# Performance work log

Measured on AMD Instinct MI355X. Metric: run time of the kernel, lower is better.

## Reference

```python
import jax, jax.numpy as jnp
import numpy as np

D, N_T, N, N_H = 8, 2048, 64, 8
STD_E = 0.02
STD_Q = 0.02


def setup_inputs() -> dict:
    key = jax.random.key(0)
    k1, k2, k3 = jax.random.split(key, 3)
    r_prime = jax.random.normal(k1, (D, N_T, N), dtype=jnp.float32)
    Q = jax.random.normal(k2, (N_H, N, N), dtype=jnp.float32) * STD_Q
    E = jax.random.normal(k3, (N_H, N, N), dtype=jnp.float32) * STD_E
    return {"r_prime": r_prime, "Q": Q, "E": E}


def reference(r_prime, Q, E):
    # r_prime: (b=d, t=n_t, i=n); Q, E: (h, i, j)
    n_t = r_prime.shape[1]
    # Omega[b,h,t,u] = sum_ij r'[b,t,i] Q[h,i,j] r'[b,u,j]
    Qr = jnp.einsum('hij,buj->bhui', Q, r_prime)          # (b, h, u, i)
    Omega = jnp.einsum('bti,bhui->bhtu', r_prime, Qr)     # (b, h, t, u)
    # causal lower-triangular mask (t >= u)
    mask = jnp.tril(jnp.ones((n_t, n_t), dtype=r_prime.dtype))
    Omega = Omega * mask  # broadcast over (b, h)
    # r[b,t,i] = sum_{h,u,j} Omega[b,h,t,u] E[h,i,j] r'[b,u,j]
    Er = jnp.einsum('hij,buj->bhui', E, r_prime)          # (b, h, u, i)
    r = jnp.einsum('bhtu,bhui->bti', Omega, Er)           # (b, t, i)
    return r
```

## Files before the change

kernel.cpp:

```cpp
#include <hip/hip_runtime.h>

#define D_B 8
#define N_T 2048
#define NN  64
#define N_H 8
#define N_C 32
#define NP  72

typedef __bf16 bf16;
typedef bf16 bf16x8 __attribute__((ext_vector_type(8)));
typedef bf16 bf16x4 __attribute__((ext_vector_type(4)));
typedef float f32x4 __attribute__((ext_vector_type(4)));

static __device__ __forceinline__ f32x4 mfma16(bf16x8 a, bf16x8 b, f32x4 c) {
    return __builtin_amdgcn_mfma_f32_16x16x32_bf16(a, b, c, 0, 0, 0);
}

static __device__ __forceinline__ bf16x8 ldcvt8(const float* p) {
    const f32x4 v0 = *(const f32x4*)p;
    const f32x4 v1 = *(const f32x4*)(p + 4);
    bf16x8 r;
#pragma unroll
    for (int k = 0; k < 4; k++) { r[k] = (bf16)v0[k]; r[4 + k] = (bf16)v1[k]; }
    return r;
}

__global__ __launch_bounds__(256, 3) void k_dg(
    const float* __restrict__ rp, const float* __restrict__ Qm,
    const float* __restrict__ Em,
    bf16* __restrict__ dGq, bf16* __restrict__ Rbf,
    bf16* __restrict__ Qrd, bf16* __restrict__ Erd)
{
    __shared__ bf16 Rl[64 * NP];
    __shared__ bf16 Ql[64 * NP];
    __shared__ bf16 El[64 * NP];
    __shared__ bf16 QT[64 * NP];
    __shared__ bf16 ET[64 * NP];
    const int b = blockIdx.x, c = blockIdx.y, qt = blockIdx.z;
    const int tid = threadIdx.x;
    const int w = tid >> 6, l = tid & 63, q = l >> 4, l16 = l & 15;
    const int row = tid >> 2, col = (tid & 3) * 16;

    {
        const float* src = rp + ((size_t)b * N_T + c * 64 + row) * NN + col;
        const bf16x8 v0 = ldcvt8(src), v1 = ldcvt8(src + 8);
        *(bf16x8*)&Rl[row * NP + col] = v0;
        *(bf16x8*)&Rl[row * NP + col + 8] = v1;
        if (qt == 0) {
            bf16* d = Rbf + ((size_t)b * N_T + c * 64 + row) * NN + col;
            *(bf16x8*)d = v0;
            *(bf16x8*)(d + 8) = v1;
        }
    }
    __syncthreads();
    const bf16x8 a0 = *(const bf16x8*)&Rl[(w * 16 + l16) * NP + q * 8];
    const bf16x8 a1 = *(const bf16x8*)&Rl[(w * 16 + l16) * NP + 32 + q * 8];

    f32x4 dacc[4];
#pragma unroll
    for (int ns = 0; ns < 4; ns++) { f32x4 z = {0.f, 0.f, 0.f, 0.f}; dacc[ns] = z; }

    for (int hh = 0; hh < 2; hh++) {
        const int h = qt * 2 + hh;
        {
            const float* qs = Qm + (size_t)h * 4096 + row * 64 + col;
            const float* es = Em + (size_t)h * 4096 + row * 64 + col;
            *(bf16x8*)&Ql[row * NP + col]     = ldcvt8(qs);
            *(bf16x8*)&Ql[row * NP + col + 8] = ldcvt8(qs + 8);
            *(bf16x8*)&El[row * NP + col]     = ldcvt8(es);
            *(bf16x8*)&El[row * NP + col + 8] = ldcvt8(es + 8);
        }
        __syncthreads();
        const size_t tb = (((size_t)(b * N_C + c)) * N_H + h) * 4096;
#pragma unroll
        for (int ns = 0; ns < 4; ns++) {
            bf16x8 b0 = *(const bf16x8*)&Ql[(ns * 16 + l16) * NP + q * 8];
            bf16x8 b1 = *(const bf16x8*)&Ql[(ns * 16 + l16) * NP + 32 + q * 8];
            f32x4 z = {0.f, 0.f, 0.f, 0.f};
            f32x4 s = mfma16(a0, b0, z);
            s = mfma16(a1, b1, s);
            bf16x4 p;
#pragma unroll
            for (int r = 0; r < 4; r++) p[r] = (bf16)s[r];
#pragma unroll
            for (int r = 0; r < 4; r++)
                Qrd[tb + (w * 16 + q * 4 + r) * 64 + ns * 16 + l16] = p[r];
            *(bf16x4*)&QT[(ns * 16 + l16) * NP + w * 16 + q * 4] = p;
            b0 = *(const bf16x8*)&El[(ns * 16 + l16) * NP + q * 8];
            b1 = *(const bf16x8*)&El[(ns * 16 + l16) * NP + 32 + q * 8];
            f32x4 s2 = mfma16(a0, b0, z);
            s2 = mfma16(a1, b1, s2);
#pragma unroll
            for (int r = 0; r < 4; r++) p[r] = (bf16)s2[r];
            *(bf16x4*)&ET[(ns * 16 + l16) * NP + w * 16 + q * 4] = p;
        }
        __syncthreads();
        {
            const bf16x8 qa0 = *(const bf16x8*)&QT[(w * 16 + l16) * NP + q * 8];
            const bf16x8 qa1 = *(const bf16x8*)&QT[(w * 16 + l16) * NP + 32 + q * 8];
#pragma unroll
            for (int ns = 0; ns < 4; ns++) {
                const bf16x8 e0 = *(const bf16x8*)&ET[(ns * 16 + l16) * NP + q * 8];
                const bf16x8 e1 = *(const bf16x8*)&ET[(ns * 16 + l16) * NP + 32 + q * 8];
                dacc[ns] = mfma16(qa0, e0, dacc[ns]);
                dacc[ns] = mfma16(qa1, e1, dacc[ns]);
            }
        }
        {
            const bf16x8 v0 = *(const bf16x8*)&ET[row * NP + col];
            const bf16x8 v1 = *(const bf16x8*)&ET[row * NP + col + 8];
            bf16* d = Erd + tb + row * 64 + col;
            *(bf16x8*)d = v0;
            *(bf16x8*)(d + 8) = v1;
        }
        __syncthreads();
    }
#pragma unroll
    for (int ns = 0; ns < 4; ns++) {
        bf16x4 p;
#pragma unroll
        for (int r = 0; r < 4; r++) p[r] = (bf16)dacc[ns][r];
        *(bf16x4*)&QT[(ns * 16 + l16) * NP + w * 16 + q * 4] = p;
    }
    __syncthreads();
    {
        bf16* dst = dGq + (((size_t)(b * N_C + c)) * 4 + qt) * 4096 + row * 64 + col;
        *(bf16x8*)dst       = *(const bf16x8*)&QT[row * NP + col];
        *(bf16x8*)(dst + 8) = *(const bf16x8*)&QT[row * NP + col + 8];
    }
}

__global__ __launch_bounds__(256, 4) void k_fold(const bf16* __restrict__ dGq,
                                                 bf16* __restrict__ dG8)
{
    const int b = blockIdx.x, c = blockIdx.y;
    const size_t base = ((size_t)(b * N_C + c)) * 4 * 4096 + threadIdx.x * 16;
    float s[16];
#pragma unroll
    for (int k = 0; k < 16; k++) s[k] = 0.f;
#pragma unroll
    for (int qt = 0; qt < 4; qt++) {
        const bf16x8 v0 = *(const bf16x8*)(dGq + base + (size_t)qt * 4096);
        const bf16x8 v1 = *(const bf16x8*)(dGq + base + (size_t)qt * 4096 + 8);
#pragma unroll
        for (int k = 0; k < 8; k++) { s[k] += (float)v0[k]; s[8 + k] += (float)v1[k]; }
    }
    bf16x8 o0, o1;
#pragma unroll
    for (int k = 0; k < 8; k++) { o0[k] = (bf16)s[k]; o1[k] = (bf16)s[8 + k]; }
    bf16* dst = dG8 + (size_t)(b * N_C + c) * 4096 + threadIdx.x * 16;
    *(bf16x8*)dst = o0;
    *(bf16x8*)(dst + 8) = o1;
}

__global__ __launch_bounds__(256, 4) void k_out(
    const bf16* __restrict__ dG8, const bf16* __restrict__ Rbf,
    const bf16* __restrict__ Qrd, const bf16* __restrict__ Erd,
    float* __restrict__ out)
{
    __shared__ bf16 Gb[64 * NP];
    __shared__ bf16 Sl[4 * 16 * NP];
    __shared__ float Ob[32 * 65];
    const int b = blockIdx.x, c = blockIdx.y, half = blockIdx.z;
    const int tid = threadIdx.x;
    const int w = tid >> 6, l = tid & 63, q = l >> 4, l16 = l & 15;
    const int s = w & 1, g = w >> 1;

    {
        float run[16];
#pragma unroll
        for (int k = 0; k < 16; k++) run[k] = 0.f;
        const bf16* base = dG8 + (size_t)b * N_C * 4096 + tid * 16;
        for (int cp = 0; cp < c; cp++) {
            const bf16x8 v0 = *(const bf16x8*)(base + (size_t)cp * 4096);
            const bf16x8 v1 = *(const bf16x8*)(base + (size_t)cp * 4096 + 8);
#pragma unroll
            for (int k = 0; k < 8; k++) { run[k] += (float)v0[k]; run[8 + k] += (float)v1[k]; }
        }
        bf16x8 o0, o1;
#pragma unroll
        for (int k = 0; k < 8; k++) { o0[k] = (bf16)run[k]; o1[k] = (bf16)run[8 + k]; }
        *(bf16x8*)&Gb[(tid >> 2) * NP + (tid & 3) * 16] = o0;
        *(bf16x8*)&Gb[(tid >> 2) * NP + (tid & 3) * 16 + 8] = o1;
    }
    __syncthreads();

    const int trow = c * 64 + half * 32 + s * 16 + l16;
    const bf16x8 ra0 = *(const bf16x8*)&Rbf[((size_t)b * N_T + trow) * NN + q * 8];
    const bf16x8 ra1 = *(const bf16x8*)&Rbf[((size_t)b * N_T + trow) * NN + 32 + q * 8];

    bf16* Sw = Sl + w * 16 * NP;
    const int NU = half ? 4 : 2;
    f32x4 acc[4];
#pragma unroll
    for (int ns = 0; ns < 4; ns++) { f32x4 z = {0.f, 0.f, 0.f, 0.f}; acc[ns] = z; }

    for (int hh = 0; hh < 4; hh++) {
        const int h = g * 4 + hh;
        const bf16* Qh = Qrd + (((size_t)(b * N_C + c)) * N_H + h) * 4096;
        const bf16* Eh = Erd + (((size_t)(b * N_C + c)) * N_H + h) * 4096;
        for (int nu = 0; nu < NU; nu++) {
            const bf16x8 b0 = *(const bf16x8*)&Qh[(nu * 16 + l16) * 64 + q * 8];
            const bf16x8 b1 = *(const bf16x8*)&Qh[(nu * 16 + l16) * 64 + 32 + q * 8];
            f32x4 z = {0.f, 0.f, 0.f, 0.f};
            f32x4 sv = mfma16(ra0, b0, z);
            sv = mfma16(ra1, b1, sv);
            const int u_loc = nu * 16 + l16;
#pragma unroll
            for (int r = 0; r < 4; r++) {
                const int t_loc = half * 32 + s * 16 + q * 4 + r;
                Sw[(q * 4 + r) * NP + u_loc] = (u_loc <= t_loc) ? (bf16)sv[r] : (bf16)0.f;
            }
        }
        const bf16x8 sa0 = *(const bf16x8*)&Sw[l16 * NP + q * 8];
#pragma unroll
        for (int ns = 0; ns < 4; ns++) {
            const bf16x8 e0 = *(const bf16x8*)&Eh[(ns * 16 + l16) * 64 + q * 8];
            acc[ns] = mfma16(sa0, e0, acc[ns]);
        }
        if (half) {
            const bf16x8 sa1 = *(const bf16x8*)&Sw[l16 * NP + 32 + q * 8];
#pragma unroll
            for (int ns = 0; ns < 4; ns++) {
                const bf16x8 e1 = *(const bf16x8*)&Eh[(ns * 16 + l16) * 64 + 32 + q * 8];
                acc[ns] = mfma16(sa1, e1, acc[ns]);
            }
        }
    }
    if (g == 1) {
#pragma unroll
        for (int ns = 0; ns < 4; ns++) {
            const bf16x8 g0 = *(const bf16x8*)&Gb[(ns * 16 + l16) * NP + q * 8];
            const bf16x8 g1 = *(const bf16x8*)&Gb[(ns * 16 + l16) * NP + 32 + q * 8];
            acc[ns] = mfma16(ra0, g0, acc[ns]);
            acc[ns] = mfma16(ra1, g1, acc[ns]);
        }
    }
    if (g == 0) {
#pragma unroll
        for (int ns = 0; ns < 4; ns++)
#pragma unroll
            for (int r = 0; r < 4; r++)
                Ob[(s * 16 + q * 4 + r) * 65 + ns * 16 + l16] = acc[ns][r];
    }
    __syncthreads();
    if (g == 1) {
        const int t0 = c * 64 + half * 32;
#pragma unroll
        for (int ns = 0; ns < 4; ns++)
#pragma unroll
            for (int r = 0; r < 4; r++) {
                const float sum = acc[ns][r] + Ob[(s * 16 + q * 4 + r) * 65 + ns * 16 + l16];
                out[((size_t)b * N_T + t0 + s * 16 + q * 4 + r) * NN + ns * 16 + l16] = sum;
            }
    }
}

extern "C" void kernel_launch(void* const* d_in, const int* in_sizes, int n_in,
                              void* d_out, int out_size, void* d_ws, size_t ws_size,
                              hipStream_t stream) {
    const float* rp = (const float*)d_in[0];
    const float* Qm = (const float*)d_in[1];
    const float* Em = (const float*)d_in[2];
    float* out = (float*)d_out;

    bf16* dGq = (bf16*)d_ws;
    bf16* Rbf = dGq + (size_t)D_B * N_C * 4 * 4096;
    bf16* Qrd = Rbf + (size_t)D_B * N_T * NN;
    bf16* Erd = Qrd + (size_t)D_B * N_C * N_H * 4096;
    bf16* dG8 = Erd + (size_t)D_B * N_C * N_H * 4096;

    k_dg<<<dim3(D_B, N_C, 4), 256, 0, stream>>>(rp, Qm, Em, dGq, Rbf, Qrd, Erd);
    k_fold<<<dim3(D_B, N_C), 256, 0, stream>>>(dGq, dG8);
    k_out<<<dim3(D_B, N_C, 2), 256, 0, stream>>>(dG8, Rbf, Qrd, Erd, out);
}
```

Before: 107.6 us.

## Process four heads per block, drop fold kernel, coalesce Qr stores via LDS

Each k_dg block now handles four heads instead of two, which halves the number of partial dG chunks. The separate k_fold kernel is removed, and k_out instead sums 2*c partials directly in its prefix loop. Qr results are staged in a new LDS tile and written out as coalesced 16-byte rows rather than scattered scalar bf16 stores. The trade-offs are fewer k_dg blocks with lower occupancy (launch bounds 3 to 2, plus extra LDS) and a doubled prefix-sum read loop in k_out.

```diff
diff --git a/kernel.cpp b/kernel.cpp
--- a/kernel.cpp
+++ b/kernel.cpp
@@ -25,7 +25,7 @@
     return r;
 }
 
-__global__ __launch_bounds__(256, 3) void k_dg(
+__global__ __launch_bounds__(256, 2) void k_dg(
     const float* __restrict__ rp, const float* __restrict__ Qm,
     const float* __restrict__ Em,
     bf16* __restrict__ dGq, bf16* __restrict__ Rbf,
@@ -36,6 +36,7 @@
     __shared__ bf16 El[64 * NP];
     __shared__ bf16 QT[64 * NP];
     __shared__ bf16 ET[64 * NP];
+    __shared__ bf16 QU[64 * NP];
     const int b = blockIdx.x, c = blockIdx.y, qt = blockIdx.z;
     const int tid = threadIdx.x;
     const int w = tid >> 6, l = tid & 63, q = l >> 4, l16 = l & 15;
@@ -60,8 +61,8 @@
 #pragma unroll
     for (int ns = 0; ns < 4; ns++) { f32x4 z = {0.f, 0.f, 0.f, 0.f}; dacc[ns] = z; }
 
-    for (int hh = 0; hh < 2; hh++) {
-        const int h = qt * 2 + hh;
+    for (int hh = 0; hh < 4; hh++) {
+        const int h = qt * 4 + hh;
         {
             const float* qs = Qm + (size_t)h * 4096 + row * 64 + col;
             const float* es = Em + (size_t)h * 4096 + row * 64 + col;
@@ -82,10 +83,10 @@
             bf16x4 p;
 #pragma unroll
             for (int r = 0; r < 4; r++) p[r] = (bf16)s[r];
+            *(bf16x4*)&QT[(ns * 16 + l16) * NP + w * 16 + q * 4] = p;
 #pragma unroll
             for (int r = 0; r < 4; r++)
-                Qrd[tb + (w * 16 + q * 4 + r) * 64 + ns * 16 + l16] = p[r];
-            *(bf16x4*)&QT[(ns * 16 + l16) * NP + w * 16 + q * 4] = p;
+                QU[(w * 16 + q * 4 + r) * NP + ns * 16 + l16] = p[r];
             b0 = *(const bf16x8*)&El[(ns * 16 + l16) * NP + q * 8];
             b1 = *(const bf16x8*)&El[(ns * 16 + l16) * NP + 32 + q * 8];
             f32x4 s2 = mfma16(a0, b0, z);
@@ -107,11 +108,12 @@
             }
         }
         {
-            const bf16x8 v0 = *(const bf16x8*)&ET[row * NP + col];
-            const bf16x8 v1 = *(const bf16x8*)&ET[row * NP + col + 8];
-            bf16* d = Erd + tb + row * 64 + col;
-            *(bf16x8*)d = v0;
-            *(bf16x8*)(d + 8) = v1;
+            bf16* de = Erd + tb + row * 64 + col;
+            *(bf16x8*)de       = *(const bf16x8*)&ET[row * NP + col];
+            *(bf16x8*)(de + 8) = *(const bf16x8*)&ET[row * NP + col + 8];
+            bf16* dq = Qrd + tb + row * 64 + col;
+            *(bf16x8*)dq       = *(const bf16x8*)&QU[row * NP + col];
+            *(bf16x8*)(dq + 8) = *(const bf16x8*)&QU[row * NP + col + 8];
         }
         __syncthreads();
     }
@@ -124,37 +126,14 @@
     }
     __syncthreads();
     {
-        bf16* dst = dGq + (((size_t)(b * N_C + c)) * 4 + qt) * 4096 + row * 64 + col;
+        bf16* dst = dGq + (((size_t)(b * N_C + c)) * 2 + qt) * 4096 + row * 64 + col;
         *(bf16x8*)dst       = *(const bf16x8*)&QT[row * NP + col];
         *(bf16x8*)(dst + 8) = *(const bf16x8*)&QT[row * NP + col + 8];
     }
 }
 
-__global__ __launch_bounds__(256, 4) void k_fold(const bf16* __restrict__ dGq,
-                                                 bf16* __restrict__ dG8)
-{
-    const int b = blockIdx.x, c = blockIdx.y;
-    const size_t base = ((size_t)(b * N_C + c)) * 4 * 4096 + threadIdx.x * 16;
-    float s[16];
-#pragma unroll
-    for (int k = 0; k < 16; k++) s[k] = 0.f;
-#pragma unroll
-    for (int qt = 0; qt < 4; qt++) {
-        const bf16x8 v0 = *(const bf16x8*)(dGq + base + (size_t)qt * 4096);
-        const bf16x8 v1 = *(const bf16x8*)(dGq + base + (size_t)qt * 4096 + 8);
-#pragma unroll
-        for (int k = 0; k < 8; k++) { s[k] += (float)v0[k]; s[8 + k] += (float)v1[k]; }
-    }
-    bf16x8 o0, o1;
-#pragma unroll
-    for (int k = 0; k < 8; k++) { o0[k] = (bf16)s[k]; o1[k] = (bf16)s[8 + k]; }
-    bf16* dst = dG8 + (size_t)(b * N_C + c) * 4096 + threadIdx.x * 16;
-    *(bf16x8*)dst = o0;
-    *(bf16x8*)(dst + 8) = o1;
-}
-
 __global__ __launch_bounds__(256, 4) void k_out(
-    const bf16* __restrict__ dG8, const bf16* __restrict__ Rbf,
+    const bf16* __restrict__ dGq, const bf16* __restrict__ Rbf,
     const bf16* __restrict__ Qrd, const bf16* __restrict__ Erd,
     float* __restrict__ out)
 {
@@ -170,10 +149,10 @@
         float run[16];
 #pragma unroll
         for (int k = 0; k < 16; k++) run[k] = 0.f;
-        const bf16* base = dG8 + (size_t)b * N_C * 4096 + tid * 16;
-        for (int cp = 0; cp < c; cp++) {
-            const bf16x8 v0 = *(const bf16x8*)(base + (size_t)cp * 4096);
-            const bf16x8 v1 = *(const bf16x8*)(base + (size_t)cp * 4096 + 8);
+        const bf16* base = dGq + (size_t)b * N_C * 2 * 4096 + tid * 16;
+        for (int t = 0; t < 2 * c; t++) {
+            const bf16x8 v0 = *(const bf16x8*)(base + (size_t)t * 4096);
+            const bf16x8 v1 = *(const bf16x8*)(base + (size_t)t * 4096 + 8);
 #pragma unroll
             for (int k = 0; k < 8; k++) { run[k] += (float)v0[k]; run[8 + k] += (float)v1[k]; }
         }
@@ -265,12 +244,10 @@
     float* out = (float*)d_out;
 
     bf16* dGq = (bf16*)d_ws;
-    bf16* Rbf = dGq + (size_t)D_B * N_C * 4 * 4096;
+    bf16* Rbf = dGq + (size_t)D_B * N_C * 2 * 4096;
     bf16* Qrd = Rbf + (size_t)D_B * N_T * NN;
     bf16* Erd = Qrd + (size_t)D_B * N_C * N_H * 4096;
-    bf16* dG8 = Erd + (size_t)D_B * N_C * N_H * 4096;
-
-    k_dg<<<dim3(D_B, N_C, 4), 256, 0, stream>>>(rp, Qm, Em, dGq, Rbf, Qrd, Erd);
-    k_fold<<<dim3(D_B, N_C), 256, 0, stream>>>(dGq, dG8);
-    k_out<<<dim3(D_B, N_C, 2), 256, 0, stream>>>(dG8, Rbf, Qrd, Erd, out);
-}
+
+    k_dg<<<dim3(D_B, N_C, 2), 256, 0, stream>>>(rp, Qm, Em, dGq, Rbf, Qrd, Erd);
+    k_out<<<dim3(D_B, N_C, 2), 256, 0, stream>>>(dGq, Rbf, Qrd, Erd, out);
+}
```

New measurement: 110.6 us. +2.8%, slower.

## Drop shared-memory staging of r' tile and overlap prefix-sum loads with MFMA work

Applied to the files above, without the earlier changes.

In k_dg the r' tile is no longer staged through shared memory. Each wave loads its MFMA A-fragments straight from global memory, which removes one LDS buffer and one barrier, and the launch bound is raised to allow 4 blocks per CU. In k_out the prefix sum over earlier chunks' dG is unrolled four-wide and issued before the per-head MFMA loop. Its LDS write and barrier are merged with the Ob partial-sum barrier, so the global loads can overlap compute and one barrier goes away. The cost is more live registers (16 floats of run state held across the MFMA loop) and some redundant global reads of r'.

```diff
diff --git a/kernel.cpp b/kernel.cpp
--- a/kernel.cpp
+++ b/kernel.cpp
@@ -25,13 +25,12 @@
     return r;
 }
 
-__global__ __launch_bounds__(256, 3) void k_dg(
+__global__ __launch_bounds__(256, 4) void k_dg(
     const float* __restrict__ rp, const float* __restrict__ Qm,
     const float* __restrict__ Em,
     bf16* __restrict__ dGq, bf16* __restrict__ Rbf,
     bf16* __restrict__ Qrd, bf16* __restrict__ Erd)
 {
-    __shared__ bf16 Rl[64 * NP];
     __shared__ bf16 Ql[64 * NP];
     __shared__ bf16 El[64 * NP];
     __shared__ bf16 QT[64 * NP];
@@ -41,20 +40,16 @@
     const int w = tid >> 6, l = tid & 63, q = l >> 4, l16 = l & 15;
     const int row = tid >> 2, col = (tid & 3) * 16;
 
-    {
+    const float* rrow = rp + ((size_t)b * N_T + c * 64 + w * 16 + l16) * NN;
+    const bf16x8 a0 = ldcvt8(rrow + q * 8);
+    const bf16x8 a1 = ldcvt8(rrow + 32 + q * 8);
+
+    if (qt == 0) {
         const float* src = rp + ((size_t)b * N_T + c * 64 + row) * NN + col;
-        const bf16x8 v0 = ldcvt8(src), v1 = ldcvt8(src + 8);
-        *(bf16x8*)&Rl[row * NP + col] = v0;
-        *(bf16x8*)&Rl[row * NP + col + 8] = v1;
-        if (qt == 0) {
-            bf16* d = Rbf + ((size_t)b * N_T + c * 64 + row) * NN + col;
-            *(bf16x8*)d = v0;
-            *(bf16x8*)(d + 8) = v1;
-        }
-    }
-    __syncthreads();
-    const bf16x8 a0 = *(const bf16x8*)&Rl[(w * 16 + l16) * NP + q * 8];
-    const bf16x8 a1 = *(const bf16x8*)&Rl[(w * 16 + l16) * NP + 32 + q * 8];
+        bf16* d = Rbf + ((size_t)b * N_T + c * 64 + row) * NN + col;
+        *(bf16x8*)d       = ldcvt8(src);
+        *(bf16x8*)(d + 8) = ldcvt8(src + 8);
+    }
 
     f32x4 dacc[4];
 #pragma unroll
@@ -166,28 +161,38 @@
     const int w = tid >> 6, l = tid & 63, q = l >> 4, l16 = l & 15;
     const int s = w & 1, g = w >> 1;
 
-    {
-        float run[16];
-#pragma unroll
-        for (int k = 0; k < 16; k++) run[k] = 0.f;
-        const bf16* base = dG8 + (size_t)b * N_C * 4096 + tid * 16;
-        for (int cp = 0; cp < c; cp++) {
-            const bf16x8 v0 = *(const bf16x8*)(base + (size_t)cp * 4096);
-            const bf16x8 v1 = *(const bf16x8*)(base + (size_t)cp * 4096 + 8);
-#pragma unroll
-            for (int k = 0; k < 8; k++) { run[k] += (float)v0[k]; run[8 + k] += (float)v1[k]; }
-        }
-        bf16x8 o0, o1;
-#pragma unroll
-        for (int k = 0; k < 8; k++) { o0[k] = (bf16)run[k]; o1[k] = (bf16)run[8 + k]; }
-        *(bf16x8*)&Gb[(tid >> 2) * NP + (tid & 3) * 16] = o0;
-        *(bf16x8*)&Gb[(tid >> 2) * NP + (tid & 3) * 16 + 8] = o1;
-    }
-    __syncthreads();
-
     const int trow = c * 64 + half * 32 + s * 16 + l16;
     const bf16x8 ra0 = *(const bf16x8*)&Rbf[((size_t)b * N_T + trow) * NN + q * 8];
     const bf16x8 ra1 = *(const bf16x8*)&Rbf[((size_t)b * N_T + trow) * NN + 32 + q * 8];
+
+    float run[16];
+#pragma unroll
+    for (int k = 0; k < 16; k++) run[k] = 0.f;
+    {
+        const bf16* base = dG8 + (size_t)b * N_C * 4096 + tid * 16;
+        int t = 0;
+        for (; t + 4 <= c; t += 4) {
+            bf16x8 v[4][2];
+#pragma unroll
+            for (int j = 0; j < 4; j++) {
+                v[j][0] = *(const bf16x8*)(base + (size_t)(t + j) * 4096);
+                v[j][1] = *(const bf16x8*)(base + (size_t)(t + j) * 4096 + 8);
+            }
+#pragma unroll
+            for (int j = 0; j < 4; j++)
+#pragma unroll
+                for (int k = 0; k < 8; k++) {
+                    run[k] += (float)v[j][0][k];
+                    run[8 + k] += (float)v[j][1][k];
+                }
+        }
+        for (; t < c; t++) {
+            const bf16x8 v0 = *(const bf16x8*)(base + (size_t)t * 4096);
+            const bf16x8 v1 = *(const bf16x8*)(base + (size_t)t * 4096 + 8);
+#pragma unroll
+            for (int k = 0; k < 8; k++) { run[k] += (float)v0[k]; run[8 + k] += (float)v1[k]; }
+        }
+    }
 
     bf16* Sw = Sl + w * 16 * NP;
     const int NU = half ? 4 : 2;
@@ -227,6 +232,22 @@
             }
         }
     }
+
+    {
+        bf16x8 o0, o1;
+#pragma unroll
+        for (int k = 0; k < 8; k++) { o0[k] = (bf16)run[k]; o1[k] = (bf16)run[8 + k]; }
+        *(bf16x8*)&Gb[(tid >> 2) * NP + (tid & 3) * 16] = o0;
+        *(bf16x8*)&Gb[(tid >> 2) * NP + (tid & 3) * 16 + 8] = o1;
+    }
+    if (g == 0) {
+#pragma unroll
+        for (int ns = 0; ns < 4; ns++)
+#pragma unroll
+            for (int r = 0; r < 4; r++)
+                Ob[(s * 16 + q * 4 + r) * 65 + ns * 16 + l16] = acc[ns][r];
+    }
+    __syncthreads();
     if (g == 1) {
 #pragma unroll
         for (int ns = 0; ns < 4; ns++) {
@@ -235,16 +256,6 @@
             acc[ns] = mfma16(ra0, g0, acc[ns]);
             acc[ns] = mfma16(ra1, g1, acc[ns]);
         }
-    }
-    if (g == 0) {
-#pragma unroll
-        for (int ns = 0; ns < 4; ns++)
-#pragma unroll
-            for (int r = 0; r < 4; r++)
-                Ob[(s * 16 + q * 4 + r) * 65 + ns * 16 + l16] = acc[ns][r];
-    }
-    __syncthreads();
-    if (g == 1) {
         const int t0 = c * 64 + half * 32;
 #pragma unroll
         for (int ns = 0; ns < 4; ns++)
```

Measured after the change: 103.3 us. 1.04x faster.
